# Optimization experiments

Hardware: AMD Instinct MI355X
Metric: run time of the kernel (lower is better)

The kernel has to match this reference:

```python
import jax, jax.numpy as jnp
import numpy as np

N = 50000       # num nodes
E = 400000      # num edges (before self loops)
IN, HID, H, OUT = 128, 64, 4, 64
SLOPE = 0.2     # PyG GATv2Conv default negative_slope


def setup_inputs() -> dict:
    key = jax.random.key(0)
    ks = jax.random.split(key, 14)
    def lin(k, fan_in, fan_out):
        return jax.random.normal(k, (fan_in, fan_out), jnp.float32) / np.sqrt(fan_in)
    return {
        "x": jax.random.normal(ks[0], (N, IN), jnp.float32),
        "edge_index": jax.random.randint(ks[1], (2, E), 0, N, jnp.int32),
        # layer 1: in=IN -> HID per head, H heads, concat
        "Wl1": lin(ks[2], IN, H * HID), "bl1": jnp.zeros((H * HID,), jnp.float32),
        "Wr1": lin(ks[3], IN, H * HID), "br1": jnp.zeros((H * HID,), jnp.float32),
        "att1": jax.random.normal(ks[4], (H, HID), jnp.float32) / np.sqrt(HID),
        "bias1": jnp.zeros((H * HID,), jnp.float32),
        # layer 2: in=H*HID -> OUT, 1 head, concat=False
        "Wl2": lin(ks[5], H * HID, OUT), "bl2": jnp.zeros((OUT,), jnp.float32),
        "Wr2": lin(ks[6], H * HID, OUT), "br2": jnp.zeros((OUT,), jnp.float32),
        "att2": jax.random.normal(ks[7], (1, OUT), jnp.float32) / np.sqrt(OUT),
        "bias2": jnp.zeros((OUT,), jnp.float32),
    }


def gatv2_conv(x, src, dst, Wl, bl, Wr, br, att, heads, out_ch, num_nodes):
    """PyG GATv2Conv (share_weights=False). src->dst aggregation at dst."""
    xl = (x @ Wl + bl).reshape(-1, heads, out_ch)  # source transform (x_j)
    xr = (x @ Wr + br).reshape(-1, heads, out_ch)  # target transform (x_i)
    m = xl[src] + xr[dst]                          # [E, H, C]
    e = jnp.sum(jax.nn.leaky_relu(m, SLOPE) * att, axis=-1)  # [E, H]
    # segment softmax over incoming edges of each dst node
    emax = jax.ops.segment_max(e, dst, num_segments=num_nodes)
    ex = jnp.exp(e - emax[dst])
    denom = jax.ops.segment_sum(ex, dst, num_segments=num_nodes)
    alpha = ex / denom[dst]                        # [E, H]
    out = jax.ops.segment_sum(alpha[:, :, None] * xl[src], dst, num_segments=num_nodes)
    return out  # [N, H, C]


def reference(x, edge_index, Wl1, bl1, Wr1, br1, att1, bias1,
              Wl2, bl2, Wr2, br2, att2, bias2):
    n = x.shape[0]
    loops = jnp.arange(n, dtype=edge_index.dtype)
    src = jnp.concatenate([edge_index[0], loops])  # add_self_loops=True
    dst = jnp.concatenate([edge_index[1], loops])
    h = gatv2_conv(x, src, dst, Wl1, bl1, Wr1, br1, att1, H, HID, n)
    h = h.reshape(n, H * HID) + bias1              # concat=True
    h = jax.nn.elu(h)                              # dropout=0.0
    o = gatv2_conv(h, src, dst, Wl2, bl2, Wr2, br2, att2, 1, OUT, n)
    return o.reshape(n, OUT) + bias2               # concat=False, heads=1
```

## Files before the change

kernel.cpp:

```cpp
#include <hip/hip_runtime.h>
#include <hip/hip_bf16.h>

typedef unsigned short u16;
typedef __attribute__((ext_vector_type(8))) short short8;
typedef __attribute__((ext_vector_type(4))) float floatx4;
typedef __attribute__((ext_vector_type(2))) float f32x2;

#define N_NODES 50000
#define N_EDGES 400000
#define ET      450000
#define F_IN    128
#define C1      256
#define HID     64
#define OUTC    64
#define SLOPE   0.2f
#define LIN1_BLOCKS 782
#define LOG2E   1.44269504089f

#if __has_builtin(__builtin_amdgcn_exp2f)
#define EXP2(x) __builtin_amdgcn_exp2f(x)
#else
#define EXP2(x) __expf((x) * 0.69314718056f)
#endif

__device__ __forceinline__ float bf2f(u16 v) {
    return __uint_as_float(((unsigned)v) << 16);
}
__device__ __forceinline__ float bflo(unsigned u) { return __uint_as_float(u << 16); }
__device__ __forceinline__ float bfhi(unsigned u) { return __uint_as_float(u & 0xffff0000u); }
__device__ __forceinline__ u16 f2bf(float f) {
    unsigned u = __float_as_uint(f);
    return (u16)((u + 0x7fffu + ((u >> 16) & 1u)) >> 16);
}
__device__ __forceinline__ f32x2 up2(unsigned u) {
    f32x2 r; r.x = bflo(u); r.y = bfhi(u); return r;
}
template<int CTRL>
__device__ __forceinline__ float dpp_add(float x) {
    return x + __int_as_float(__builtin_amdgcn_update_dpp(
        0, __float_as_int(x), CTRL, 0xF, 0xF, true));
}
__device__ __forceinline__ float red16(float p) {
    p = dpp_add<0xB1>(p);
    p = dpp_add<0x4E>(p);
    p = dpp_add<0x141>(p);
    p = dpp_add<0x140>(p);
    return p;
}
template<int CTRL>
__device__ __forceinline__ f32x2 dpp_add2(f32x2 x) {
    f32x2 o;
    o.x = __int_as_float(__builtin_amdgcn_update_dpp(
        0, __float_as_int(x.x), CTRL, 0xF, 0xF, true));
    o.y = __int_as_float(__builtin_amdgcn_update_dpp(
        0, __float_as_int(x.y), CTRL, 0xF, 0xF, true));
    return x + o;
}
__device__ __forceinline__ f32x2 red16x2(f32x2 p) {
    p = dpp_add2<0xB1>(p);
    p = dpp_add2<0x4E>(p);
    p = dpp_add2<0x141>(p);
    p = dpp_add2<0x140>(p);
    return p;
}
__device__ __forceinline__ bool detect_f32(const unsigned* __restrict__ xw) {
    unsigned w = xw[threadIdx.x & 63];
    unsigned aexp = (w >> 7) & 0xFFu;
    unsigned long long b = __ballot(aexp >= 170u || aexp <= 40u);
    return __popcll(b) >= 16;
}

__global__ __launch_bounds__(256) void convert_all_kernel(
    const unsigned* __restrict__ xw,
    const void* wl1, const void* wr1, const void* wl2, const void* wr2,
    const void* s0, const void* s1, const void* s2, const void* s3,
    const void* s4, const void* s5, const void* s6, const void* s7,
    u16* __restrict__ wt, u16* __restrict__ prm, int* __restrict__ hist)
{
    if (blockIdx.x >= 385) {
        int idx = (blockIdx.x - 385) * 256 + threadIdx.x;
        if (idx < N_NODES) hist[idx] = 0;
        return;
    }
    bool f32m = detect_f32(xw);
    if (blockIdx.x == 384) {
        for (int t = threadIdx.x; t < 1280; t += 256) {
            const void* src; int local;
            if      (t < 256)  { src = s0; local = t; }
            else if (t < 512)  { src = s1; local = t - 256; }
            else if (t < 768)  { src = s2; local = t - 512; }
            else if (t < 1024) { src = s3; local = t - 768; }
            else if (t < 1088) { src = s4; local = t - 1024; }
            else if (t < 1152) { src = s5; local = t - 1088; }
            else if (t < 1216) { src = s6; local = t - 1152; }
            else               { src = s7; local = t - 1216; }
            prm[t] = f32m ? f2bf(((const float*)src)[local]) : ((const u16*)src)[local];
        }
        return;
    }
    int t = blockIdx.x * 256 + threadIdx.x;
    const void* src; int local, k, n, K, base;
    if (t < 32768)      { src = wl1; local = t;         k = local >> 8; n = local & 255; K = 128; base = 0; }
    else if (t < 65536) { src = wr1; local = t - 32768; k = local >> 8; n = local & 255; K = 128; base = 32768; }
    else if (t < 81920) { src = wl2; local = t - 65536; k = local >> 6; n = local & 63;  K = 256; base = 65536; }
    else                { src = wr2; local = t - 81920; k = local >> 6; n = local & 63;  K = 256; base = 81920; }
    u16 v = f32m ? f2bf(((const float*)src)[local]) : ((const u16*)src)[local];
    wt[base + n * K + k] = v;
}

__global__ __launch_bounds__(256) void scan1_kernel(const int* __restrict__ hist,
                                                    int* __restrict__ rowptr,
                                                    int* __restrict__ bsum)
{
    int t = threadIdx.x;
    int i = blockIdx.x * 256 + t;
    int v = (i < N_NODES) ? hist[i] : 0;
    __shared__ int sd[256];
    sd[t] = v;
    __syncthreads();
    #pragma unroll
    for (int ofs = 1; ofs < 256; ofs <<= 1) {
        int u = (t >= ofs) ? sd[t - ofs] : 0;
        __syncthreads();
        sd[t] += u;
        __syncthreads();
    }
    if (i < N_NODES) rowptr[i] = sd[t] - v;
    if (t == 255) bsum[blockIdx.x] = sd[255];
}

__global__ __launch_bounds__(256) void scan3_kernel(int* __restrict__ rowptr,
                                                    const int* __restrict__ bsum,
                                                    int* __restrict__ off)
{
    int t = threadIdx.x;
    int v = (t < (int)blockIdx.x) ? bsum[t] : 0;
    __shared__ int sd[256];
    sd[t] = v;
    __syncthreads();
    #pragma unroll
    for (int ofs = 1; ofs < 256; ofs <<= 1) {
        int u = (t >= ofs) ? sd[t - ofs] : 0;
        __syncthreads();
        sd[t] += u;
        __syncthreads();
    }
    int boff = sd[255];
    int i = blockIdx.x * 256 + t;
    if (i < N_NODES) {
        int r = rowptr[i] + boff;
        rowptr[i] = r;
        off[i] = r;
    }
}

__global__ __launch_bounds__(256) void scatter_kernel(const int* __restrict__ ei,
                                                      int* __restrict__ off,
                                                      int* __restrict__ src_csr)
{
    int t = blockIdx.x * 256 + threadIdx.x;
    if (t >= ET) return;
    int s, d;
    if (t < N_EDGES) { s = ei[t]; d = ei[N_EDGES + t]; } else { s = d = t - N_EDGES; }
    int pos = atomicAdd(&off[d], 1);
    src_csr[pos] = s;
}

__global__ __launch_bounds__(256) void lin1_hist_kernel(
    const u16* __restrict__ X, const u16* __restrict__ Wt,
    const u16* __restrict__ bl, const u16* __restrict__ br,
    u16* __restrict__ Yl, u16* __restrict__ Yr, int nrows,
    const int* __restrict__ ei, int* __restrict__ hist)
{
    constexpr int K = 128, N = 256, LS = K + 8;
    __shared__ __align__(16) u16 sX[64 * LS];
    __shared__ __align__(16) u16 sW[64 * LS];

    if (blockIdx.x >= LIN1_BLOCKS) {
        int t = (blockIdx.x - LIN1_BLOCKS) * 256 + threadIdx.x;
        if (t < ET) {
            int d = (t < N_EDGES) ? ei[N_EDGES + t] : t - N_EDGES;
            atomicAdd(&hist[d], 1);
        }
        return;
    }

    const bool f32m = detect_f32((const unsigned*)X);
    const float* X32 = (const float*)X;
    const int row0 = blockIdx.x * 64;
    const int wave = threadIdx.x >> 6, lane = threadIdx.x & 63;
    const int quad = lane >> 4, l16 = lane & 15;

    for (int i = threadIdx.x * 8; i < 64 * K; i += 2048) {
        int r = i >> 7, c = i & 127;
        int gr = row0 + r;
        u16* dst = &sX[r * LS + c];
        if (f32m) {
            float4 v0 = make_float4(0.f, 0.f, 0.f, 0.f), v1 = v0;
            if (gr < nrows) {
                v0 = *(const float4*)&X32[(size_t)gr * K + c];
                v1 = *(const float4*)&X32[(size_t)gr * K + c + 4];
            }
            ushort4 p0, p1;
            p0.x = f2bf(v0.x); p0.y = f2bf(v0.y); p0.z = f2bf(v0.z); p0.w = f2bf(v0.w);
            p1.x = f2bf(v1.x); p1.y = f2bf(v1.y); p1.z = f2bf(v1.z); p1.w = f2bf(v1.w);
            *(ushort4*)dst = p0;
            *(ushort4*)(dst + 4) = p1;
        } else {
            uint4 v = {0u, 0u, 0u, 0u};
            if (gr < nrows) v = *(const uint4*)&X[(size_t)gr * K + c];
            *(uint4*)dst = v;
        }
    }
    __syncthreads();

    short8 a[4];
    #pragma unroll
    for (int kk = 0; kk < 4; ++kk)
        a[kk] = *(const short8*)&sX[(wave * 16 + l16) * LS + kk * 32 + quad * 8];

    for (int side = 0; side < 2; ++side) {
        const u16* wbase = Wt + side * (N * K);
        const u16* bias  = side ? br : bl;
        u16* Y = side ? Yr : Yl;
        for (int ch = 0; ch < 4; ++ch) {
            __syncthreads();
            for (int i = threadIdx.x * 8; i < 64 * K; i += 2048) {
                int n = i >> 7, c = i & 127;
                *(uint4*)&sW[n * LS + c] = *(const uint4*)&wbase[(size_t)(ch * 64 + n) * K + c];
            }
            __syncthreads();
            floatx4 acc0 = {0.f, 0.f, 0.f, 0.f}, acc1 = acc0, acc2 = acc0, acc3 = acc0;
            #pragma unroll
            for (int kk = 0; kk < 4; ++kk) {
                short8 b0 = *(const short8*)&sW[(l16) * LS + kk * 32 + quad * 8];
                short8 b1 = *(const short8*)&sW[(16 + l16) * LS + kk * 32 + quad * 8];
                short8 b2 = *(const short8*)&sW[(32 + l16) * LS + kk * 32 + quad * 8];
                short8 b3 = *(const short8*)&sW[(48 + l16) * LS + kk * 32 + quad * 8];
                acc0 = __builtin_amdgcn_mfma_f32_16x16x32_bf16(a[kk], b0, acc0, 0, 0, 0);
                acc1 = __builtin_amdgcn_mfma_f32_16x16x32_bf16(a[kk], b1, acc1, 0, 0, 0);
                acc2 = __builtin_amdgcn_mfma_f32_16x16x32_bf16(a[kk], b2, acc2, 0, 0, 0);
                acc3 = __builtin_amdgcn_mfma_f32_16x16x32_bf16(a[kk], b3, acc3, 0, 0, 0);
            }
            const int rbase = row0 + wave * 16 + quad * 4;
            #pragma unroll
            for (int cf = 0; cf < 4; ++cf) {
                const floatx4 av = (cf == 0) ? acc0 : (cf == 1) ? acc1 : (cf == 2) ? acc2 : acc3;
                const int col = ch * 64 + cf * 16 + l16;
                const float bv = bf2f(bias[col]);
                #pragma unroll
                for (int r = 0; r < 4; ++r) {
                    int row = rbase + r;
                    if (row < nrows) Y[(size_t)row * N + col] = f2bf(av[r] + bv);
                }
            }
        }
    }
}

__global__ __launch_bounds__(256) void lin2_fused_kernel(
    const u16* __restrict__ X, const u16* __restrict__ Wt,
    const u16* __restrict__ bl, const u16* __restrict__ br,
    u16* __restrict__ Yl, u16* __restrict__ Yr, int nrows)
{
    constexpr int K = 256, N = 64, LS = K + 8;
    __shared__ __align__(16) u16 sX[64 * LS];
    __shared__ __align__(16) u16 sW[64 * LS];
    const int row0 = blockIdx.x * 64;
    const int wave = threadIdx.x >> 6, lane = threadIdx.x & 63;
    const int quad = lane >> 4, l16 = lane & 15;

    for (int i = threadIdx.x * 8; i < 64 * K; i += 2048) {
        int r = i >> 8, c = i & 255;
        int gr = row0 + r;
        uint4 v = {0u, 0u, 0u, 0u};
        if (gr < nrows) v = *(const uint4*)&X[(size_t)gr * K + c];
        *(uint4*)&sX[r * LS + c] = v;
    }
    __syncthreads();

    short8 a[8];
    #pragma unroll
    for (int kk = 0; kk < 8; ++kk)
        a[kk] = *(const short8*)&sX[(wave * 16 + l16) * LS + kk * 32 + quad * 8];

    for (int side = 0; side < 2; ++side) {
        const u16* wbase = Wt + side * (N * K);
        const u16* bias  = side ? br : bl;
        u16* Y = side ? Yr : Yl;
        __syncthreads();
        for (int i = threadIdx.x * 8; i < 64 * K; i += 2048) {
            int n = i >> 8, c = i & 255;
            *(uint4*)&sW[n * LS + c] = *(const uint4*)&wbase[(size_t)n * K + c];
        }
        __syncthreads();
        floatx4 acc0 = {0.f, 0.f, 0.f, 0.f}, acc1 = acc0, acc2 = acc0, acc3 = acc0;
        #pragma unroll
        for (int kk = 0; kk < 8; ++kk) {
            short8 b0 = *(const short8*)&sW[(l16) * LS + kk * 32 + quad * 8];
            short8 b1 = *(const short8*)&sW[(16 + l16) * LS + kk * 32 + quad * 8];
            short8 b2 = *(const short8*)&sW[(32 + l16) * LS + kk * 32 + quad * 8];
            short8 b3 = *(const short8*)&sW[(48 + l16) * LS + kk * 32 + quad * 8];
            acc0 = __builtin_amdgcn_mfma_f32_16x16x32_bf16(a[kk], b0, acc0, 0, 0, 0);
            acc1 = __builtin_amdgcn_mfma_f32_16x16x32_bf16(a[kk], b1, acc1, 0, 0, 0);
            acc2 = __builtin_amdgcn_mfma_f32_16x16x32_bf16(a[kk], b2, acc2, 0, 0, 0);
            acc3 = __builtin_amdgcn_mfma_f32_16x16x32_bf16(a[kk], b3, acc3, 0, 0, 0);
        }
        const int rbase = row0 + wave * 16 + quad * 4;
        #pragma unroll
        for (int cf = 0; cf < 4; ++cf) {
            const floatx4 av = (cf == 0) ? acc0 : (cf == 1) ? acc1 : (cf == 2) ? acc2 : acc3;
            const int col = cf * 16 + l16;
            const float bv = bf2f(bias[col]);
            #pragma unroll
            for (int r = 0; r < 4; ++r) {
                int row = rbase + r;
                if (row < nrows) Y[(size_t)row * N + col] = f2bf(av[r] + bv);
            }
        }
    }
}

__global__ __launch_bounds__(64, 6) void node1_kernel(
    const u16* __restrict__ xl, const u16* __restrict__ xr,
    const int* __restrict__ rowptr, const int* __restrict__ hist,
    const int* __restrict__ src_csr, const u16* __restrict__ att,
    const u16* __restrict__ bias, u16* __restrict__ hout)
{
    const int d = blockIdx.x;
    const int l = threadIdx.x;
    const int start = rowptr[d];
    const int deg = hist[d];
    const u16* __restrict__ xlp = xl + l * 4;

    uint2 auv = *(const uint2*)&att[l * 4];
    const f32x2 atA = up2(auv.x) * LOG2E, atB = up2(auv.y) * LOG2E;
    uint2 ruv = *(const uint2*)&xr[(size_t)d * C1 + l * 4];
    const f32x2 rA = up2(ruv.x), rB = up2(ruv.y);

    float m = -1e30f, la = 0.f;
    f32x2 accA = {0.f, 0.f}, accB = {0.f, 0.f};

    int s0 = src_csr[start];
    int s1 = (1 < deg) ? src_csr[start + 1] : s0;
    int s2 = (2 < deg) ? src_csr[start + 2] : s0;
    int s3 = (3 < deg) ? src_csr[start + 3] : s0;
    uint2 u0 = *(const uint2*)&xlp[(size_t)s0 * C1];
    uint2 u1 = *(const uint2*)&xlp[(size_t)s1 * C1];
    uint2 u2 = *(const uint2*)&xlp[(size_t)s2 * C1];
    uint2 u3 = *(const uint2*)&xlp[(size_t)s3 * C1];

    for (int j = 0; j < deg; j += 4) {
        const uint2 c0 = u0, c1 = u1, c2 = u2, c3 = u3;
        const bool v1 = j + 1 < deg, v2 = j + 2 < deg, v3 = j + 3 < deg;
        const int jn = j + 4;
        if (jn < deg) {
            int t0 = src_csr[start + jn];
            int t1 = (jn + 1 < deg) ? src_csr[start + jn + 1] : t0;
            int t2 = (jn + 2 < deg) ? src_csr[start + jn + 2] : t0;
            int t3 = (jn + 3 < deg) ? src_csr[start + jn + 3] : t0;
            u0 = *(const uint2*)&xlp[(size_t)t0 * C1];
            u1 = *(const uint2*)&xlp[(size_t)t1 * C1];
            u2 = *(const uint2*)&xlp[(size_t)t2 * C1];
            u3 = *(const uint2*)&xlp[(size_t)t3 * C1];
        }
        f32x2 x0A = up2(c0.x), x0B = up2(c0.y);
        f32x2 x1A = up2(c1.x), x1B = up2(c1.y);
        f32x2 x2A = up2(c2.x), x2B = up2(c2.y);
        f32x2 x3A = up2(c3.x), x3B = up2(c3.y);
        f32x2 t, pv;
        t = x0A + rA; t = __builtin_elementwise_max(t, t * SLOPE); pv  = t * atA;
        t = x0B + rB; t = __builtin_elementwise_max(t, t * SLOPE); pv += t * atB;
        float p0 = pv.x + pv.y;
        t = x1A + rA; t = __builtin_elementwise_max(t, t * SLOPE); pv  = t * atA;
        t = x1B + rB; t = __builtin_elementwise_max(t, t * SLOPE); pv += t * atB;
        float p1 = pv.x + pv.y;
        t = x2A + rA; t = __builtin_elementwise_max(t, t * SLOPE); pv  = t * atA;
        t = x2B + rB; t = __builtin_elementwise_max(t, t * SLOPE); pv += t * atB;
        float p2 = pv.x + pv.y;
        t = x3A + rA; t = __builtin_elementwise_max(t, t * SLOPE); pv  = t * atA;
        t = x3B + rB; t = __builtin_elementwise_max(t, t * SLOPE); pv += t * atB;
        float p3 = pv.x + pv.y;
        f32x2 P01 = {p0, p1}, P23 = {p2, p3};
        P01 = red16x2(P01);
        P23 = red16x2(P23);
        p0 = P01.x; p1 = P01.y; p2 = P23.x; p3 = P23.y;
        float pm = p0;
        if (v1) pm = fmaxf(pm, p1);
        if (v2) pm = fmaxf(pm, p2);
        if (v3) pm = fmaxf(pm, p3);
        float mn = fmaxf(m, pm);
        float sc = EXP2(m - mn);
        float w0 = EXP2(p0 - mn);
        float w1 = v1 ? EXP2(p1 - mn) : 0.f;
        float w2 = v2 ? EXP2(p2 - mn) : 0.f;
        float w3 = v3 ? EXP2(p3 - mn) : 0.f;
        la = la * sc + w0 + w1 + w2 + w3;
        accA = accA * sc + x0A * w0 + x1A * w1 + x2A * w2 + x3A * w3;
        accB = accB * sc + x0B * w0 + x1B * w1 + x2B * w2 + x3B * w3;
        m = mn;
    }
    const float inv = 1.f / la;
    const int c = l * 4;
    float v0 = accA.x * inv + bf2f(bias[c + 0]);
    float v1 = accA.y * inv + bf2f(bias[c + 1]);
    float v2 = accB.x * inv + bf2f(bias[c + 2]);
    float v3 = accB.y * inv + bf2f(bias[c + 3]);
    v0 = v0 > 0.f ? v0 : __expf(fminf(v0, 0.f)) - 1.f;
    v1 = v1 > 0.f ? v1 : __expf(fminf(v1, 0.f)) - 1.f;
    v2 = v2 > 0.f ? v2 : __expf(fminf(v2, 0.f)) - 1.f;
    v3 = v3 > 0.f ? v3 : __expf(fminf(v3, 0.f)) - 1.f;
    ushort4 o;
    o.x = f2bf(v0); o.y = f2bf(v1); o.z = f2bf(v2); o.w = f2bf(v3);
    *(ushort4*)&hout[(size_t)d * C1 + c] = o;
}

__global__ __launch_bounds__(64, 8) void node2_kernel(
    const u16* __restrict__ xl, const u16* __restrict__ xr,
    const int* __restrict__ rowptr, const int* __restrict__ hist,
    const int* __restrict__ src_csr, const u16* __restrict__ att,
    const u16* __restrict__ bias, void* __restrict__ outp,
    const unsigned* __restrict__ xorig)
{
    const bool f32o = detect_f32(xorig);
    const int d = blockIdx.x;
    const int l = threadIdx.x;
    const int start = rowptr[d];
    const int deg = hist[d];
    const int g = l >> 4, sub = l & 15;
    const int c0 = sub * 4;
    const u16* __restrict__ xlp = xl + c0;

    uint2 auv = *(const uint2*)&att[c0];
    const f32x2 atA = up2(auv.x) * LOG2E, atB = up2(auv.y) * LOG2E;
    uint2 ruv = *(const uint2*)&xr[(size_t)d * OUTC + c0];
    const f32x2 rA = up2(ruv.x), rB = up2(ruv.y);

    float m = -1e30f, la = 0.f;
    f32x2 accA = {0.f, 0.f}, accB = {0.f, 0.f};

    int sN = (g < deg) ? src_csr[start + g] : d;
    uint2 uN = *(const uint2*)&xlp[(size_t)sN * OUTC];

    for (int j = 0; j < deg; j += 4) {
        const bool valid = j + g < deg;
        const uint2 uv = uN;
        const int jn = j + 4;
        if (jn < deg) {
            int sn = (jn + g < deg) ? src_csr[start + jn + g] : d;
            uN = *(const uint2*)&xlp[(size_t)sn * OUTC];
        }
        f32x2 xA = up2(uv.x), xB = up2(uv.y);
        f32x2 t, pv;
        t = xA + rA; t = __builtin_elementwise_max(t, t * SLOPE); pv  = t * atA;
        t = xB + rB; t = __builtin_elementwise_max(t, t * SLOPE); pv += t * atB;
        float p = pv.x + pv.y;
        p = red16(p);
        float pvv = valid ? p : -1e30f;
        float mn = fmaxf(m, pvv);
        float sc = EXP2(m - mn);
        float w  = valid ? EXP2(p - mn) : 0.f;
        la = la * sc + w;
        accA = accA * sc + xA * w;
        accB = accB * sc + xB * w;
        m = mn;
    }
    #pragma unroll
    for (int ofs = 16; ofs <= 32; ofs <<= 1) {
        float mo = __shfl_xor(m, ofs);
        float lo = __shfl_xor(la, ofs);
        float bax = __shfl_xor(accA.x, ofs);
        float bay = __shfl_xor(accA.y, ofs);
        float bbx = __shfl_xor(accB.x, ofs);
        float bby = __shfl_xor(accB.y, ofs);
        float mn = fmaxf(m, mo);
        float e0 = EXP2(m - mn), e1 = EXP2(mo - mn);
        la = la * e0 + lo * e1;
        accA.x = accA.x * e0 + bax * e1;
        accA.y = accA.y * e0 + bay * e1;
        accB.x = accB.x * e0 + bbx * e1;
        accB.y = accB.y * e0 + bby * e1;
        m = mn;
    }
    if (g == 0) {
        const float inv = 1.f / la;
        float v0 = accA.x * inv + bf2f(bias[c0 + 0]);
        float v1 = accA.y * inv + bf2f(bias[c0 + 1]);
        float v2 = accB.x * inv + bf2f(bias[c0 + 2]);
        float v3 = accB.y * inv + bf2f(bias[c0 + 3]);
        if (f32o) {
            float4 o = make_float4(v0, v1, v2, v3);
            *(float4*)&((float*)outp)[(size_t)d * OUTC + c0] = o;
        } else {
            ushort4 o;
            o.x = f2bf(v0); o.y = f2bf(v1); o.z = f2bf(v2); o.w = f2bf(v3);
            *(ushort4*)&((u16*)outp)[(size_t)d * OUTC + c0] = o;
        }
    }
}

extern "C" void kernel_launch(void* const* d_in, const int* in_sizes, int n_in,
                              void* d_out, int out_size, void* d_ws, size_t ws_size,
                              hipStream_t stream)
{
    const void* x  = d_in[0];
    const int*  ei = (const int*)d_in[1];

    char* ws = (char*)d_ws;
    u16* xl1     = (u16*)(ws + 0);
    u16* xr1     = (u16*)(ws + 25600000);
    u16* hbuf    = (u16*)(ws + 51200000);
    u16* xl2     = (u16*)(ws + 0);
    u16* xr2     = (u16*)(ws + 6400000);
    int* hist    = (int*)(ws + 76800000);
    int* rowptr  = (int*)(ws + 77000000);
    int* off     = (int*)(ws + 77200000);
    int* src_csr = (int*)(ws + 77400000);
    u16* prm     = (u16*)(ws + 79200064);
    u16* wt      = (u16*)(ws + 79210240);
    int* bsum    = (int*)(ws + 79410000);

    u16* bl1   = prm + 0;
    u16* br1   = prm + 256;
    u16* att1  = prm + 512;
    u16* bias1 = prm + 768;
    u16* bl2   = prm + 1024;
    u16* br2   = prm + 1088;
    u16* att2  = prm + 1152;
    u16* bias2 = prm + 1216;
    u16* wt1   = wt + 0;
    u16* wt2   = wt + 65536;

    convert_all_kernel<<<581, 256, 0, stream>>>(
        (const unsigned*)x,
        d_in[2], d_in[4], d_in[8], d_in[10],
        d_in[3], d_in[5], d_in[6], d_in[7], d_in[9], d_in[11], d_in[12], d_in[13],
        wt, prm, hist);

    const int eb = (ET + 255) / 256;
    lin1_hist_kernel<<<LIN1_BLOCKS + eb, 256, 0, stream>>>(
        (const u16*)x, wt1, bl1, br1, xl1, xr1, N_NODES, ei, hist);

    scan1_kernel<<<196, 256, 0, stream>>>(hist, rowptr, bsum);
    scan3_kernel<<<196, 256, 0, stream>>>(rowptr, bsum, off);
    scatter_kernel<<<eb, 256, 0, stream>>>(ei, off, src_csr);

    node1_kernel<<<N_NODES, 64, 0, stream>>>(xl1, xr1, rowptr, hist, src_csr, att1, bias1, hbuf);
    lin2_fused_kernel<<<(N_NODES + 63) / 64, 256, 0, stream>>>(hbuf, wt2, bl2, br2, xl2, xr2, N_NODES);
    node2_kernel<<<N_NODES, 64, 0, stream>>>(xl2, xr2, rowptr, hist, src_csr, att2, bias2, d_out,
                                             (const unsigned*)x);
}
```

Measured before the change: 239.4 us.

## Enlarge lin1 row tile, deepen node2 prefetch, skip redundant softmax rescales

The lin1 GEMM block now covers 128 rows instead of 64, so each weight tile loaded into shared memory is reused by twice as many MFMA ops. Node kernels clamp CSR indices instead of branching and only rescale the online-softmax accumulators when the running max actually increases. node1 splits out the partial tail group, and node2 prefetches two groups ahead. The trade-offs are more registers and LDS per lin1 block, fewer lin1 blocks in flight, and a wave-level vote branch in the softmax loops.

```diff
diff --git a/kernel.cpp b/kernel.cpp
--- a/kernel.cpp
+++ b/kernel.cpp
@@ -14,7 +14,7 @@
 #define HID     64
 #define OUTC    64
 #define SLOPE   0.2f
-#define LIN1_BLOCKS 782
+#define LIN1_BLOCKS 391
 #define LOG2E   1.44269504089f
 
 #if __has_builtin(__builtin_amdgcn_exp2f)
@@ -172,8 +172,8 @@
     u16* __restrict__ Yl, u16* __restrict__ Yr, int nrows,
     const int* __restrict__ ei, int* __restrict__ hist)
 {
-    constexpr int K = 128, N = 256, LS = K + 8;
-    __shared__ __align__(16) u16 sX[64 * LS];
+    constexpr int K = 128, N = 256, LS = K + 8, RB = 128;
+    __shared__ __align__(16) u16 sX[RB * LS];
     __shared__ __align__(16) u16 sW[64 * LS];
 
     if (blockIdx.x >= LIN1_BLOCKS) {
@@ -187,11 +187,11 @@
 
     const bool f32m = detect_f32((const unsigned*)X);
     const float* X32 = (const float*)X;
-    const int row0 = blockIdx.x * 64;
+    const int row0 = blockIdx.x * RB;
     const int wave = threadIdx.x >> 6, lane = threadIdx.x & 63;
     const int quad = lane >> 4, l16 = lane & 15;
 
-    for (int i = threadIdx.x * 8; i < 64 * K; i += 2048) {
+    for (int i = threadIdx.x * 8; i < RB * K; i += 2048) {
         int r = i >> 7, c = i & 127;
         int gr = row0 + r;
         u16* dst = &sX[r * LS + c];
@@ -214,10 +214,12 @@
     }
     __syncthreads();
 
-    short8 a[4];
+    short8 a[2][4];
     #pragma unroll
-    for (int kk = 0; kk < 4; ++kk)
-        a[kk] = *(const short8*)&sX[(wave * 16 + l16) * LS + kk * 32 + quad * 8];
+    for (int t = 0; t < 2; ++t)
+        #pragma unroll
+        for (int kk = 0; kk < 4; ++kk)
+            a[t][kk] = *(const short8*)&sX[(wave * 32 + t * 16 + l16) * LS + kk * 32 + quad * 8];
 
     for (int side = 0; side < 2; ++side) {
         const u16* wbase = Wt + side * (N * K);
@@ -230,28 +232,39 @@
                 *(uint4*)&sW[n * LS + c] = *(const uint4*)&wbase[(size_t)(ch * 64 + n) * K + c];
             }
             __syncthreads();
-            floatx4 acc0 = {0.f, 0.f, 0.f, 0.f}, acc1 = acc0, acc2 = acc0, acc3 = acc0;
+            floatx4 acc[2][4];
+            #pragma unroll
+            for (int t = 0; t < 2; ++t)
+                #pragma unroll
+                for (int cf = 0; cf < 4; ++cf)
+                    acc[t][cf] = (floatx4){0.f, 0.f, 0.f, 0.f};
             #pragma unroll
             for (int kk = 0; kk < 4; ++kk) {
                 short8 b0 = *(const short8*)&sW[(l16) * LS + kk * 32 + quad * 8];
                 short8 b1 = *(const short8*)&sW[(16 + l16) * LS + kk * 32 + quad * 8];
                 short8 b2 = *(const short8*)&sW[(32 + l16) * LS + kk * 32 + quad * 8];
                 short8 b3 = *(const short8*)&sW[(48 + l16) * LS + kk * 32 + quad * 8];
-                acc0 = __builtin_amdgcn_mfma_f32_16x16x32_bf16(a[kk], b0, acc0, 0, 0, 0);
-                acc1 = __builtin_amdgcn_mfma_f32_16x16x32_bf16(a[kk], b1, acc1, 0, 0, 0);
-                acc2 = __builtin_amdgcn_mfma_f32_16x16x32_bf16(a[kk], b2, acc2, 0, 0, 0);
-                acc3 = __builtin_amdgcn_mfma_f32_16x16x32_bf16(a[kk], b3, acc3, 0, 0, 0);
+                #pragma unroll
+                for (int t = 0; t < 2; ++t) {
+                    acc[t][0] = __builtin_amdgcn_mfma_f32_16x16x32_bf16(a[t][kk], b0, acc[t][0], 0, 0, 0);
+                    acc[t][1] = __builtin_amdgcn_mfma_f32_16x16x32_bf16(a[t][kk], b1, acc[t][1], 0, 0, 0);
+                    acc[t][2] = __builtin_amdgcn_mfma_f32_16x16x32_bf16(a[t][kk], b2, acc[t][2], 0, 0, 0);
+                    acc[t][3] = __builtin_amdgcn_mfma_f32_16x16x32_bf16(a[t][kk], b3, acc[t][3], 0, 0, 0);
+                }
             }
-            const int rbase = row0 + wave * 16 + quad * 4;
             #pragma unroll
-            for (int cf = 0; cf < 4; ++cf) {
-                const floatx4 av = (cf == 0) ? acc0 : (cf == 1) ? acc1 : (cf == 2) ? acc2 : acc3;
-                const int col = ch * 64 + cf * 16 + l16;
-                const float bv = bf2f(bias[col]);
+            for (int t = 0; t < 2; ++t) {
+                const int rbase = row0 + wave * 32 + t * 16 + quad * 4;
                 #pragma unroll
-                for (int r = 0; r < 4; ++r) {
-                    int row = rbase + r;
-                    if (row < nrows) Y[(size_t)row * N + col] = f2bf(av[r] + bv);
+                for (int cf = 0; cf < 4; ++cf) {
+                    const floatx4 av = acc[t][cf];
+                    const int col = ch * 64 + cf * 16 + l16;
+                    const float bv = bf2f(bias[col]);
+                    #pragma unroll
+                    for (int r = 0; r < 4; ++r) {
+                        int row = rbase + r;
+                        if (row < nrows) Y[(size_t)row * N + col] = f2bf(av[r] + bv);
+                    }
                 }
             }
         }
@@ -331,6 +344,7 @@
     const int l = threadIdx.x;
     const int start = rowptr[d];
     const int deg = hist[d];
+    const int dm1 = deg - 1;
     const u16* __restrict__ xlp = xl + l * 4;
 
     uint2 auv = *(const uint2*)&att[l * 4];
@@ -342,23 +356,23 @@
     f32x2 accA = {0.f, 0.f}, accB = {0.f, 0.f};
 
     int s0 = src_csr[start];
-    int s1 = (1 < deg) ? src_csr[start + 1] : s0;
-    int s2 = (2 < deg) ? src_csr[start + 2] : s0;
-    int s3 = (3 < deg) ? src_csr[start + 3] : s0;
+    int s1 = src_csr[start + min(1, dm1)];
+    int s2 = src_csr[start + min(2, dm1)];
+    int s3 = src_csr[start + min(3, dm1)];
     uint2 u0 = *(const uint2*)&xlp[(size_t)s0 * C1];
     uint2 u1 = *(const uint2*)&xlp[(size_t)s1 * C1];
     uint2 u2 = *(const uint2*)&xlp[(size_t)s2 * C1];
     uint2 u3 = *(const uint2*)&xlp[(size_t)s3 * C1];
 
-    for (int j = 0; j < deg; j += 4) {
+    int j = 0;
+    for (; j + 4 <= deg; j += 4) {
         const uint2 c0 = u0, c1 = u1, c2 = u2, c3 = u3;
-        const bool v1 = j + 1 < deg, v2 = j + 2 < deg, v3 = j + 3 < deg;
         const int jn = j + 4;
         if (jn < deg) {
             int t0 = src_csr[start + jn];
-            int t1 = (jn + 1 < deg) ? src_csr[start + jn + 1] : t0;
-            int t2 = (jn + 2 < deg) ? src_csr[start + jn + 2] : t0;
-            int t3 = (jn + 3 < deg) ? src_csr[start + jn + 3] : t0;
+            int t1 = src_csr[start + min(jn + 1, dm1)];
+            int t2 = src_csr[start + min(jn + 2, dm1)];
+            int t3 = src_csr[start + min(jn + 3, dm1)];
             u0 = *(const uint2*)&xlp[(size_t)t0 * C1];
             u1 = *(const uint2*)&xlp[(size_t)t1 * C1];
             u2 = *(const uint2*)&xlp[(size_t)t2 * C1];
@@ -385,20 +399,55 @@
         P01 = red16x2(P01);
         P23 = red16x2(P23);
         p0 = P01.x; p1 = P01.y; p2 = P23.x; p3 = P23.y;
+        float pm = fmaxf(fmaxf(p0, p1), fmaxf(p2, p3));
+        if (__any(pm > m)) {
+            float mn = fmaxf(m, pm);
+            float sc = EXP2(m - mn);
+            la *= sc; accA *= sc; accB *= sc;
+            m = mn;
+        }
+        float w0 = EXP2(p0 - m);
+        float w1 = EXP2(p1 - m);
+        float w2 = EXP2(p2 - m);
+        float w3 = EXP2(p3 - m);
+        la += w0 + w1 + w2 + w3;
+        accA += x0A * w0 + x1A * w1 + x2A * w2 + x3A * w3;
+        accB += x0B * w0 + x1B * w1 + x2B * w2 + x3B * w3;
+    }
+    if (j < deg) {
+        const bool v1 = j + 1 < deg, v2 = j + 2 < deg;
+        f32x2 x0A = up2(u0.x), x0B = up2(u0.y);
+        f32x2 x1A = up2(u1.x), x1B = up2(u1.y);
+        f32x2 x2A = up2(u2.x), x2B = up2(u2.y);
+        f32x2 t, pv;
+        t = x0A + rA; t = __builtin_elementwise_max(t, t * SLOPE); pv  = t * atA;
+        t = x0B + rB; t = __builtin_elementwise_max(t, t * SLOPE); pv += t * atB;
+        float p0 = pv.x + pv.y;
+        t = x1A + rA; t = __builtin_elementwise_max(t, t * SLOPE); pv  = t * atA;
+        t = x1B + rB; t = __builtin_elementwise_max(t, t * SLOPE); pv += t * atB;
+        float p1 = pv.x + pv.y;
+        t = x2A + rA; t = __builtin_elementwise_max(t, t * SLOPE); pv  = t * atA;
+        t = x2B + rB; t = __builtin_elementwise_max(t, t * SLOPE); pv += t * atB;
+        float p2 = pv.x + pv.y;
+        f32x2 P01 = {p0, p1};
+        P01 = red16x2(P01);
+        p0 = P01.x; p1 = P01.y;
+        p2 = red16(p2);
         float pm = p0;
         if (v1) pm = fmaxf(pm, p1);
         if (v2) pm = fmaxf(pm, p2);
-        if (v3) pm = fmaxf(pm, p3);
-        float mn = fmaxf(m, pm);
-        float sc = EXP2(m - mn);
-        float w0 = EXP2(p0 - mn);
-        float w1 = v1 ? EXP2(p1 - mn) : 0.f;
-        float w2 = v2 ? EXP2(p2 - mn) : 0.f;
-        float w3 = v3 ? EXP2(p3 - mn) : 0.f;
-        la = la * sc + w0 + w1 + w2 + w3;
-        accA = accA * sc + x0A * w0 + x1A * w1 + x2A * w2 + x3A * w3;
-        accB = accB * sc + x0B * w0 + x1B * w1 + x2B * w2 + x3B * w3;
-        m = mn;
+        if (__any(pm > m)) {
+            float mn = fmaxf(m, pm);
+            float sc = EXP2(m - mn);
+            la *= sc; accA *= sc; accB *= sc;
+            m = mn;
+        }
+        float w0 = EXP2(p0 - m);
+        float w1 = v1 ? EXP2(p1 - m) : 0.f;
+        float w2 = v2 ? EXP2(p2 - m) : 0.f;
+        la += w0 + w1 + w2;
+        accA += x0A * w0 + x1A * w1 + x2A * w2;
+        accB += x0B * w0 + x1B * w1 + x2B * w2;
     }
     const float inv = 1.f / la;
     const int c = l * 4;
@@ -427,6 +476,7 @@
     const int l = threadIdx.x;
     const int start = rowptr[d];
     const int deg = hist[d];
+    const int dm1 = deg - 1;
     const int g = l >> 4, sub = l & 15;
     const int c0 = sub * 4;
     const u16* __restrict__ xlp = xl + c0;
@@ -439,16 +489,18 @@
     float m = -1e30f, la = 0.f;
     f32x2 accA = {0.f, 0.f}, accB = {0.f, 0.f};
 
-    int sN = (g < deg) ? src_csr[start + g] : d;
-    uint2 uN = *(const uint2*)&xlp[(size_t)sN * OUTC];
+    int sA = src_csr[start + min(g, dm1)];
+    uint2 uA = *(const uint2*)&xlp[(size_t)sA * OUTC];
+    int sB = src_csr[start + min(4 + g, dm1)];
+    uint2 uB = *(const uint2*)&xlp[(size_t)sB * OUTC];
 
     for (int j = 0; j < deg; j += 4) {
         const bool valid = j + g < deg;
-        const uint2 uv = uN;
-        const int jn = j + 4;
-        if (jn < deg) {
-            int sn = (jn + g < deg) ? src_csr[start + jn + g] : d;
-            uN = *(const uint2*)&xlp[(size_t)sn * OUTC];
+        const uint2 uv = uA;
+        uA = uB;
+        {
+            int sC = src_csr[start + min(j + 8 + g, dm1)];
+            uB = *(const uint2*)&xlp[(size_t)sC * OUTC];
         }
         f32x2 xA = up2(uv.x), xB = up2(uv.y);
         f32x2 t, pv;
@@ -457,13 +509,16 @@
         float p = pv.x + pv.y;
         p = red16(p);
         float pvv = valid ? p : -1e30f;
-        float mn = fmaxf(m, pvv);
-        float sc = EXP2(m - mn);
-        float w  = valid ? EXP2(p - mn) : 0.f;
-        la = la * sc + w;
-        accA = accA * sc + xA * w;
-        accB = accB * sc + xB * w;
-        m = mn;
+        if (__any(pvv > m)) {
+            float mn = fmaxf(m, pvv);
+            float sc = EXP2(m - mn);
+            la *= sc; accA *= sc; accB *= sc;
+            m = mn;
+        }
+        float w = valid ? EXP2(p - m) : 0.f;
+        la += w;
+        accA += xA * w;
+        accB += xB * w;
     }
     #pragma unroll
     for (int ofs = 16; ofs <= 32; ofs <<= 1) {
```

Result: slower. 249.4 us (+4.2%).
